# Kernel tuning notes

Hardware: AMD Instinct MI355X
Metric: run time of the kernel (lower is better)

Reference implementation:

```python
import jax, jax.numpy as jnp
import numpy as np
from jax.scipy.optimize import minimize

LAMDA = 0.01        # lamda default in MI()
N_DOMAINS = 2       # domain_label is binary (source/target)
MAXITER = 50        # BFGS iteration budget (torchmin l-bfgs analogue)


def _sq_dists(A, B):
    # squared euclidean pairwise distances == torch.cdist(A, B, p=2) ** 2
    an = jnp.sum(A * A, axis=-1)
    bn = jnp.sum(B * B, axis=-1)
    return an[:, None] + bn[None, :] - 2.0 * (A @ B.T)


def _median_sigma(sf):
    # sigma = median of nonzero squared pairwise source distances.
    # With continuous features the only zeros are the diagonal, so mask it.
    pd = jnp.maximum(_sq_dists(sf, sf), 0.0)
    pd = jnp.where(jnp.eye(pd.shape[0], dtype=bool), jnp.nan, pd)
    return jnp.nanmedian(pd)


def _build(sf, tf, y, l):
    # Gaussian kernel masked by class agreement, plus domain one-hots.
    sigma = _median_sigma(sf)
    X = jnp.concatenate([sf, tf], axis=0)              # [N, d]
    D = _sq_dists(X, X)                                 # [N, N]
    Deltay = (y[:, None] == y[None, :]).astype(X.dtype)
    K_W = jnp.exp(-D / sigma) * Deltay                  # [N, N]
    onehot = jax.nn.one_hot(l[:, 0], N_DOMAINS, dtype=X.dtype)  # [N, 2]
    KD = K_W * (onehot @ onehot.T)                      # K_W * Deltal
    w = jnp.sum(onehot, axis=0) / X.shape[0]            # domain counts / N
    return K_W, KD, onehot, w


def _div(theta, K_W, KD, onehot, w):
    # mean((K_W*Deltal) @ theta) - mean(exp((theta*K_W) @ Deltal - 1))
    # Deltal = onehot @ onehot.T (rank-2), so the second NxN @ NxN matmul
    # collapses to A = K_W @ (theta[:,None]*onehot) with column weights w.
    term1 = jnp.mean(KD @ theta)
    A = K_W @ (theta[:, None] * onehot)                 # [N, 2]
    term2 = jnp.mean(jnp.exp(A - 1.0) @ w)
    return term1 - term2


def _solve_theta(K_W, KD, onehot, w):
    N = K_W.shape[0]
    obj = lambda th: -_div(th, K_W, KD, onehot, w) + LAMDA * (th @ th)
    res = minimize(obj, jnp.zeros((N,), K_W.dtype), method="BFGS",
                   options={"maxiter": MAXITER})
    return res.x


def setup_inputs() -> dict:
    key = jax.random.key(0)
    k1, k2, k3, k4 = jax.random.split(key, 4)
    B, d, n_class = 2048, 256, 31
    source_features = jax.random.normal(k1, (B, d), dtype=jnp.float32)
    target_features = jax.random.normal(k2, (B, d), dtype=jnp.float32)
    y = jax.random.randint(k3, (2 * B,), 0, n_class, dtype=jnp.int32)
    l = jax.random.randint(k4, (2 * B, 1), 0, N_DOMAINS, dtype=jnp.int32)
    return {"source_features": source_features, "target_features": target_features,
            "y": y, "l": l}


def reference(source_features, target_features, y, l):
    K_W, KD, onehot, w = _build(source_features, target_features, y, l)
    theta_hat = _solve_theta(K_W, KD, onehot, w)
    return _div(theta_hat, K_W, KD, onehot, w)
```

## Files before the change

kernel.cpp:

```cpp
#include <hip/hip_runtime.h>
#include <math.h>

#define N_TOT   4096
#define N_SRC   2048
#define DIMF    256
#define NCLASS  31
#define LAMBDA  0.01f

#define K_TRI1  1048063LL
#define K_TRI2  1048064LL

#define WS_ACC    0
#define WS_HIST0  64
#define WS_HISTA  16448
#define WS_HISTB  32832
#define WS_H2A    49216
#define WS_H2B    50240
#define WS_STATE  51264
#define WS_TICK   51520
#define WS_META   52288
#define WS_SCAL   52800
#define ZERO_BYTES 53248
#define WS_PERM   53248
#define WS_XN     69632
#define WS_DS     1048576
#define WS_KBLK   17825792

#define MAXW 224
#define MAXM 112
#define WPAD 116

__device__ __forceinline__ float bf2f(unsigned short h) {
  return __uint_as_float(((unsigned)h) << 16);
}

__device__ __forceinline__ float wredF(float v) {
#pragma unroll
  for (int o = 1; o < 64; o <<= 1) v += __shfl_xor(v, o, 64);
  return v;
}

__device__ __forceinline__ double blockReduceSum(double v, double* red) {
#pragma unroll
  for (int o = 32; o > 0; o >>= 1) v += __shfl_down(v, o, 64);
  int w = threadIdx.x >> 6, lane = threadIdx.x & 63;
  __syncthreads();
  if (lane == 0) red[w] = v;
  __syncthreads();
  return red[0] + red[1] + red[2] + red[3];
}

__device__ __forceinline__ void blockReduceSumMax(double s, double mx, double* red,
                                                  double& os, double& om) {
#pragma unroll
  for (int o = 32; o > 0; o >>= 1) {
    s += __shfl_down(s, o, 64);
    double u = __shfl_down(mx, o, 64);
    mx = fmax(mx, u);
  }
  int w = threadIdx.x >> 6, lane = threadIdx.x & 63;
  __syncthreads();
  if (lane == 0) { red[w] = s; red[4 + w] = mx; }
  __syncthreads();
  os = red[0] + red[1] + red[2] + red[3];
  om = fmax(fmax(red[4], red[5]), fmax(red[6], red[7]));
}

__device__ void scan_find(const unsigned* hist, int nbins, long long k, unsigned* shOut, int tid) {
  __shared__ long long tsum[256];
  int per = nbins / 256;
  long long s = 0;
  for (int q = 0; q < per; q++) s += hist[tid * per + q];
  tsum[tid] = s;
  __syncthreads();
  long long acc = s;
  for (int off = 1; off < 256; off <<= 1) {
    long long add = (tid >= off) ? tsum[tid - off] : 0;
    __syncthreads();
    acc += add;
    tsum[tid] = acc;
    __syncthreads();
  }
  long long run = acc - s;
  for (int q = 0; q < per; q++) {
    unsigned c = hist[tid * per + q];
    if (k >= run && k < run + (long long)c) { shOut[0] = (unsigned)(tid * per + q); shOut[1] = (unsigned)(k - run); }
    run += c;
  }
  __syncthreads();
}

__global__ __launch_bounds__(256) void xn_kernel(const float* __restrict__ sf,
                                                 const float* __restrict__ tf,
                                                 float* __restrict__ xn,
                                                 uint4* __restrict__ wsz) {
  if (blockIdx.x == 0) {
    uint4 z; z.x = 0; z.y = 0; z.z = 0; z.w = 0;
    for (int q = threadIdx.x; q < ZERO_BYTES / 16; q += 256) wsz[q] = z;
  }
  int wid = threadIdx.x >> 6, lane = threadIdx.x & 63;
  int row = blockIdx.x * 4 + wid;
  const float* src = (row < N_SRC) ? (sf + (size_t)row * DIMF) : (tf + (size_t)(row - N_SRC) * DIMF);
  float4 v = ((const float4*)src)[lane];
  float s = v.x * v.x + v.y * v.y + v.z * v.z + v.w * v.w;
#pragma unroll
  for (int o = 32; o > 0; o >>= 1) s += __shfl_down(s, o, 64);
  if (lane == 0) xn[row] = s;
}

__global__ __launch_bounds__(256) void dist_k(const float* __restrict__ sf,
                                              const float* __restrict__ xn,
                                              float* __restrict__ Ds,
                                              unsigned* __restrict__ h) {
  __shared__ float As[16][68];
  __shared__ float Bs[16][68];
  __shared__ unsigned lh[2][4096];
  const int tx = threadIdx.x, ty = threadIdx.y;
  const int tid = ty * 16 + tx;
  const int par = tid & 1;
  for (int q = tid; q < 8192; q += 256) lh[q >> 12][q & 4095] = 0;
  int b = blockIdx.x;
  int by = (int)((sqrtf(8.f * (float)b + 1.f) - 1.f) * 0.5f);
  while ((by + 1) * (by + 2) / 2 <= b) ++by;
  while (by * (by + 1) / 2 > b) --by;
  int bx = b - by * (by + 1) / 2;
  const int R = by * 64, C = bx * 64;
  const int si = tid >> 2, sq = tid & 3;
  float4 va = ((const float4*)(sf + (size_t)(R + si) * 256 + 0))[sq];
  float4 vb = ((const float4*)(sf + (size_t)(C + si) * 256 + 0))[sq];
  float acc[4][4] = {};
  for (int kc = 0; kc < 256; kc += 16) {
    As[sq * 4 + 0][si] = va.x; As[sq * 4 + 1][si] = va.y; As[sq * 4 + 2][si] = va.z; As[sq * 4 + 3][si] = va.w;
    Bs[sq * 4 + 0][si] = vb.x; Bs[sq * 4 + 1][si] = vb.y; Bs[sq * 4 + 2][si] = vb.z; Bs[sq * 4 + 3][si] = vb.w;
    __syncthreads();
    if (kc + 16 < 256) {
      va = ((const float4*)(sf + (size_t)(R + si) * 256 + kc + 16))[sq];
      vb = ((const float4*)(sf + (size_t)(C + si) * 256 + kc + 16))[sq];
    }
#pragma unroll
    for (int k = 0; k < 16; k++) {
      float4 a = *(const float4*)&As[k][ty * 4];
      float4 b2 = *(const float4*)&Bs[k][tx * 4];
      acc[0][0] += a.x * b2.x; acc[0][1] += a.x * b2.y; acc[0][2] += a.x * b2.z; acc[0][3] += a.x * b2.w;
      acc[1][0] += a.y * b2.x; acc[1][1] += a.y * b2.y; acc[1][2] += a.y * b2.z; acc[1][3] += a.y * b2.w;
      acc[2][0] += a.z * b2.x; acc[2][1] += a.z * b2.y; acc[2][2] += a.z * b2.z; acc[2][3] += a.z * b2.w;
      acc[3][0] += a.w * b2.x; acc[3][1] += a.w * b2.y; acc[3][2] += a.w * b2.z; acc[3][3] += a.w * b2.w;
    }
    __syncthreads();
  }
  int jbase = C + tx * 4;
  float xnj0 = xn[jbase + 0], xnj1 = xn[jbase + 1], xnj2 = xn[jbase + 2], xnj3 = xn[jbase + 3];
#pragma unroll
  for (int r = 0; r < 4; r++) {
    int i = R + ty * 4 + r;
    float xni = xn[i];
    float v[4];
    v[0] = fmaxf(xni + xnj0 - 2.f * acc[r][0], 0.f);
    v[1] = fmaxf(xni + xnj1 - 2.f * acc[r][1], 0.f);
    v[2] = fmaxf(xni + xnj2 - 2.f * acc[r][2], 0.f);
    v[3] = fmaxf(xni + xnj3 - 2.f * acc[r][3], 0.f);
    if (jbase + 3 < i) {
      float4 o; o.x = v[0]; o.y = v[1]; o.z = v[2]; o.w = v[3];
      ((float4*)&Ds[(size_t)i * 2048 + jbase])[0] = o;
      atomicAdd(&lh[par][__float_as_uint(v[0]) >> 20], 1u);
      atomicAdd(&lh[par][__float_as_uint(v[1]) >> 20], 1u);
      atomicAdd(&lh[par][__float_as_uint(v[2]) >> 20], 1u);
      atomicAdd(&lh[par][__float_as_uint(v[3]) >> 20], 1u);
    } else {
#pragma unroll
      for (int k = 0; k < 4; k++) {
        if (jbase + k < i) {
          Ds[(size_t)i * 2048 + jbase + k] = v[k];
          atomicAdd(&lh[par][__float_as_uint(v[k]) >> 20], 1u);
        }
      }
    }
  }
  __syncthreads();
  for (int q = tid; q < 4096; q += 256) {
    unsigned v = lh[0][q] + lh[1][q];
    if (v) atomicAdd(&h[q], v);
  }
}

__global__ __launch_bounds__(256) void scan0_k(const unsigned* __restrict__ h, unsigned* __restrict__ st) {
  __shared__ unsigned r0[2];
  __shared__ unsigned r1[2];
  scan_find(h, 4096, K_TRI1, r0, threadIdx.x);
  scan_find(h, 4096, K_TRI2, r1, threadIdx.x);
  if (threadIdx.x == 0) { st[0] = r0[0]; st[1] = r0[1]; st[2] = r1[0]; st[3] = r1[1]; }
}

__global__ __launch_bounds__(256) void hist1_k(const float* __restrict__ Ds, const unsigned* __restrict__ st,
                                               unsigned* __restrict__ hA, unsigned* __restrict__ hB) {
  __shared__ unsigned lA[4096];
  __shared__ unsigned lB[4096];
  for (int i = threadIdx.x; i < 4096; i += 256) { lA[i] = 0; lB[i] = 0; }
  __syncthreads();
  unsigned s0 = st[0], s1 = st[2];
  int gw = (blockIdx.x * 256 + threadIdx.x) >> 6;
  int lane = threadIdx.x & 63;
  const float* row = Ds + (size_t)gw * 2048;
  for (int j = lane; j < gw; j += 64) {
    unsigned u = __float_as_uint(row[j]);
    unsigned hi = u >> 20, mid = (u >> 8) & 0xFFFu;
    if (hi == s0) atomicAdd(&lA[mid], 1u);
    if (hi == s1) atomicAdd(&lB[mid], 1u);
  }
  __syncthreads();
  for (int i = threadIdx.x; i < 4096; i += 256) {
    if (lA[i]) atomicAdd(&hA[i], lA[i]);
    if (lB[i]) atomicAdd(&hB[i], lB[i]);
  }
}

__global__ __launch_bounds__(256) void scan1_k(const unsigned* __restrict__ hA, const unsigned* __restrict__ hB,
                                               unsigned* __restrict__ st) {
  __shared__ unsigned r0[2];
  __shared__ unsigned r1[2];
  long long kA = (long long)st[1];
  long long kB = (long long)st[3];
  scan_find(hA, 4096, kA, r0, threadIdx.x);
  scan_find(hB, 4096, kB, r1, threadIdx.x);
  if (threadIdx.x == 0) { st[4] = r0[0]; st[5] = r0[1]; st[6] = r1[0]; st[7] = r1[1]; }
}

__global__ __launch_bounds__(256) void hist2_k(const float* __restrict__ Ds, const unsigned* __restrict__ st,
                                               unsigned* __restrict__ hA, unsigned* __restrict__ hB) {
  __shared__ unsigned lA[256];
  __shared__ unsigned lB[256];
  lA[threadIdx.x] = 0; lB[threadIdx.x] = 0;
  __syncthreads();
  unsigned p0 = (st[0] << 12) | st[4];
  unsigned p1 = (st[2] << 12) | st[6];
  int gw = (blockIdx.x * 256 + threadIdx.x) >> 6;
  int lane = threadIdx.x & 63;
  const float* row = Ds + (size_t)gw * 2048;
  for (int j = lane; j < gw; j += 64) {
    unsigned u = __float_as_uint(row[j]);
    unsigned pre = u >> 8;
    if (pre == p0) atomicAdd(&lA[u & 0xFFu], 1u);
    if (pre == p1) atomicAdd(&lB[u & 0xFFu], 1u);
  }
  __syncthreads();
  if (lA[threadIdx.x]) atomicAdd(&hA[threadIdx.x], lA[threadIdx.x]);
  if (lB[threadIdx.x]) atomicAdd(&hB[threadIdx.x], lB[threadIdx.x]);
}

__global__ __launch_bounds__(256) void scan2b_k(const unsigned* __restrict__ hA, const unsigned* __restrict__ hB,
                                                const unsigned* __restrict__ st, float* __restrict__ scal,
                                                const int* __restrict__ y, const int* __restrict__ l,
                                                int* __restrict__ perm, int* __restrict__ meta) {
  int tid = threadIdx.x;
  __shared__ unsigned r0[2];
  __shared__ unsigned r1[2];
  scan_find(hA, 256, (long long)st[5], r0, tid);
  scan_find(hB, 256, (long long)st[7], r1, tid);
  if (tid == 0) {
    unsigned v1 = (st[0] << 20) | (st[4] << 8) | r0[0];
    unsigned v2 = (st[2] << 20) | (st[6] << 8) | r1[0];
    scal[0] = 0.5f * (__uint_as_float(v1) + __uint_as_float(v2));
  }
  __shared__ unsigned cl[64];
  __shared__ unsigned bs2[64];
  __shared__ unsigned cur[64];
  if (tid < 64) cl[tid] = 0;
  __syncthreads();
  for (int i = tid; i < N_TOT; i += 256) atomicAdd(&cl[y[i] * 2 + l[i]], 1u);
  __syncthreads();
  if (tid == 0) {
    unsigned run = 0;
    for (int b2 = 0; b2 < 62; b2++) { bs2[b2] = run; run += cl[b2]; }
    unsigned run2 = 0, cnt0 = 0;
    for (int c = 0; c < NCLASS; c++) {
      int n = (int)(cl[2 * c] + cl[2 * c + 1]);
      meta[c] = n; meta[32 + c] = (int)cl[2 * c]; meta[64 + c] = (int)bs2[2 * c];
      meta[96 + c] = (int)run2; run2 += (unsigned)(n * n);
      cnt0 += cl[2 * c];
    }
    scal[1] = (float)((double)cnt0 / (4096.0 * 4096.0));
    scal[2] = (float)((double)(N_TOT - cnt0) / (4096.0 * 4096.0));
  }
  __syncthreads();
  if (tid < 64) cur[tid] = bs2[tid];
  __syncthreads();
  for (int i = tid; i < N_TOT; i += 256) {
    int b2 = y[i] * 2 + l[i];
    unsigned pos = atomicAdd(&cur[b2], 1u);
    perm[pos] = i;
  }
}

__global__ __launch_bounds__(256) void build_k(const float* __restrict__ sf, const float* __restrict__ tf,
                                               const float* __restrict__ xn, const int* __restrict__ perm,
                                               const int* __restrict__ meta, const float* __restrict__ scal,
                                               float* __restrict__ gK) {
  const int c = blockIdx.z;
  const int n = meta[c];
  const int cs = meta[64 + c];
  const int bo = meta[96 + c];
  const int T = (n + 15) >> 4;
  int b = blockIdx.x;
  if (b >= T * (T + 1) / 2) return;
  int by = (int)((sqrtf(8.f * (float)b + 1.f) - 1.f) * 0.5f);
  while ((by + 1) * (by + 2) / 2 <= b) ++by;
  while (by * (by + 1) / 2 > b) --by;
  int bx = b - by * (by + 1) / 2;
  const int i0 = by * 16, j0 = bx * 16;
  const int tx = threadIdx.x, ty = threadIdx.y;
  __shared__ float As[16][260];
  __shared__ float Bs[16][260];
  __shared__ float ot[16][17];
  __shared__ int ra[16];
  __shared__ int rb[16];
  int tid = ty * 16 + tx;
  if (tid < 16) { int il = i0 + tid; ra[tid] = (il < n) ? perm[cs + il] : -1; }
  else if (tid < 32) { int jl = j0 + tid - 16; rb[tid - 16] = (jl < n) ? perm[cs + jl] : -1; }
  __syncthreads();
  for (int e = tid; e < 1024; e += 256) {
    int r = e >> 6, q = e & 63;
    int g = ra[r];
    if (g >= 0) {
      const float* src = (g < N_SRC) ? (sf + (size_t)g * DIMF) : (tf + (size_t)(g - N_SRC) * DIMF);
      ((float4*)&As[r][q * 4])[0] = ((const float4*)src)[q];
    }
    int g2 = rb[r];
    if (g2 >= 0) {
      const float* src = (g2 < N_SRC) ? (sf + (size_t)g2 * DIMF) : (tf + (size_t)(g2 - N_SRC) * DIMF);
      ((float4*)&Bs[r][q * 4])[0] = ((const float4*)src)[q];
    }
  }
  __syncthreads();
  int il = i0 + ty, jl = j0 + tx;
  float val = 0.f;
  if (il < n && jl < n) {
    float dot = 0.f;
    const float4* a4 = (const float4*)&As[ty][0];
    const float4* b4 = (const float4*)&Bs[tx][0];
#pragma unroll 16
    for (int q = 0; q < 64; q++) {
      float4 a = a4[q], b2 = b4[q];
      dot += a.x * b2.x + a.y * b2.y + a.z * b2.z + a.w * b2.w;
    }
    int gi = ra[ty], gj = rb[tx];
    float d = xn[gi] + xn[gj] - 2.f * dot;
    val = expf(-d / scal[0]);
    gK[(size_t)bo + (size_t)il * n + jl] = val;
  }
  ot[ty][tx] = val;
  __syncthreads();
  if (by != bx) {
    int il2 = j0 + ty, jl2 = i0 + tx;
    if (il2 < n && jl2 < n) gK[(size_t)bo + (size_t)il2 * n + jl2] = ot[tx][ty];
  }
}

__global__ __launch_bounds__(256) void solver_k(const float* __restrict__ gK, const int* __restrict__ meta,
                                                const float* __restrict__ scal, double* __restrict__ acc,
                                                unsigned* __restrict__ tick, float* __restrict__ out) {
  const int c = blockIdx.x >> 1, d = blockIdx.x & 1;
  const int n = meta[c];
  const int m0 = meta[32 + c];
  const int m = d ? (n - m0) : m0;
  const int c0 = d ? m0 : 0;
  const int bo = meta[96 + c];
  const float gamma = scal[1 + d];
  const int tid = threadIdx.x;
  const int wv = tid >> 6, lane = tid & 63;

  __shared__ unsigned short Wl[MAXW * WPAD];
  __shared__ float pS[4 * MAXM];
  __shared__ float pD[4 * MAXM];
  __shared__ float Av[MAXW];
  __shared__ float Sv[MAXW];
  __shared__ float Uv[MAXW];
  __shared__ float Bq[MAXW];
  __shared__ float bc[MAXM];
  __shared__ float gv[MAXM];
  __shared__ float dgv[MAXM];
  __shared__ alignas(16) float th[128];
  __shared__ alignas(16) float pv[128];
  __shared__ alignas(16) float xv[128];
  __shared__ double red[16];
  __shared__ double gds[2];
  __shared__ int cgst[2];

  const float* K = gK + bo;
  const int st = n;
  const int mp2 = (m + 1) & ~1;
  const int mp4 = (m + 3) & ~3;
  const int iw0 = (n * wv) >> 2, iw1 = (n * (wv + 1)) >> 2;
  const int rq = tid >> 2, ql = tid & 3;

  for (int i = rq; i < n; i += 64) {
    const float* Kr = K + (size_t)i * st + c0;
    unsigned short* Wr = Wl + i * WPAD;
    for (int j = ql; j < m; j += 4) {
      unsigned u = __float_as_uint(Kr[j]);
      u += 0x7fffu + ((u >> 16) & 1u);
      Wr[j] = (unsigned short)(u >> 16);
    }
    if (ql == 0) for (int j = m; j < mp4; j++) Wr[j] = 0;
  }
  for (int j = rq; j < m; j += 64) {
    const float* Kr = K + (size_t)(c0 + j) * st + c0;
    float s = 0.f;
    for (int r = ql; r < m; r += 4) s += Kr[r];
    s += __shfl_xor(s, 1, 64);
    s += __shfl_xor(s, 2, 64);
    if (ql == 0) bc[j] = s * (1.0f / 4096.0f);
  }
  __syncthreads();
  for (int j = tid; j < 128; j += 256) { th[j] = 0.f; pv[j] = 0.f; xv[j] = 0.f; }
  __syncthreads();

  for (int it = 0; it < 25; it++) {
    double o = 0.0;
    if (it == 0) {
      const float s0c = gamma * expf(-1.f);
      for (int i = tid; i < n; i += 256) { Av[i] = 0.f; Sv[i] = s0c; o += (double)s0c; }
    } else {
      for (int i = tid; i < n; i += 256) {
        const unsigned short* Wr = Wl + i * WPAD;
        float a = 0.f;
#pragma unroll 4
        for (int j = 0; j < mp4; j += 4) {
          unsigned long long u = *(const unsigned long long*)(Wr + j);
          float4 t4 = *(const float4*)(th + j);
          unsigned lo = (unsigned)u, hi = (unsigned)(u >> 32);
          a += __uint_as_float(lo << 16) * t4.x
             + __uint_as_float(lo & 0xffff0000u) * t4.y
             + __uint_as_float(hi << 16) * t4.z
             + __uint_as_float(hi & 0xffff0000u) * t4.w;
        }
        Av[i] = a;
        float si = gamma * expf(fminf(a - 1.f, 30.f));
        Sv[i] = si; o += (double)si;
      }
      for (int j = tid; j < m; j += 256) {
        float t_ = th[j];
        o += (double)(-bc[j] * t_ + LAMBDA * t_ * t_);
      }
    }
    __syncthreads();
    if (it == 0) {
      for (int j = lane; j < m; j += 64) {
        const unsigned short* Wc = Wl + j;
        float s_ = 0.f, ds_ = 0.f;
        int i = iw0;
        for (; i + 3 < iw1; i += 4) {
          float w0 = bf2f(Wc[(i + 0) * WPAD]), w1 = bf2f(Wc[(i + 1) * WPAD]);
          float w2 = bf2f(Wc[(i + 2) * WPAD]), w3 = bf2f(Wc[(i + 3) * WPAD]);
          float a0 = w0 * Sv[i], a1 = w1 * Sv[i + 1], a2 = w2 * Sv[i + 2], a3 = w3 * Sv[i + 3];
          s_ += a0 + a1 + a2 + a3;
          ds_ += a0 * w0 + a1 * w1 + a2 * w2 + a3 * w3;
        }
        for (; i < iw1; i++) { float w = bf2f(Wc[i * WPAD]); float a = w * Sv[i]; s_ += a; ds_ += a * w; }
        pS[wv * MAXM + j] = s_; pD[wv * MAXM + j] = ds_;
      }
    } else {
      for (int j = lane; j < m; j += 64) {
        const unsigned short* Wc = Wl + j;
        float s_ = 0.f;
        int i = iw0;
        for (; i + 3 < iw1; i += 4)
          s_ += bf2f(Wc[(i+0)*WPAD]) * Sv[i]   + bf2f(Wc[(i+1)*WPAD]) * Sv[i+1]
              + bf2f(Wc[(i+2)*WPAD]) * Sv[i+2] + bf2f(Wc[(i+3)*WPAD]) * Sv[i+3];
        for (; i < iw1; i++) s_ += bf2f(Wc[i * WPAD]) * Sv[i];
        pS[wv * MAXM + j] = s_;
      }
    }
    __syncthreads();
    double gm = 0.0;
    for (int j = tid; j < m; j += 256) {
      float s_ = pS[j] + pS[MAXM + j] + pS[2 * MAXM + j] + pS[3 * MAXM + j];
      if (it == 0) {
        float ds_ = pD[j] + pD[MAXM + j] + pD[2 * MAXM + j] + pD[3 * MAXM + j];
        dgv[j] = ds_ + 2.f * LAMBDA;
      }
      float g = s_ - bc[j] + 2.f * LAMBDA * th[j];
      gv[j] = g;
      double ag = fabs((double)g); if (ag > gm) gm = ag;
    }
    double obj, gmax;
    blockReduceSumMax(o, gm, red, obj, gmax);
    if (gmax < 1e-5) break;

    const float tolf = (it == 0) ? 1e-2f : ((it == 1) ? 1e-3f : 1e-4f);
    float p0 = 0.f, p1 = 0.f, r0 = 0.f, r1 = 0.f, z0 = 0.f, z1 = 0.f, x0 = 0.f, x1 = 0.f;
    float dg0 = 1.f, dg1 = 1.f, rzf = 0.f, rz0f = 0.f;
    double gtpacc = 0.0;
    const int j0 = lane, j1 = lane + 64;
    if (wv == 0) {
      if (j0 < m) { dg0 = dgv[j0]; r0 = -gv[j0]; z0 = r0 / dg0; }
      if (j1 < m) { dg1 = dgv[j1]; r1 = -gv[j1]; z1 = r1 / dg1; }
      p0 = z0; p1 = z1;
      rzf = wredF(r0 * z0 + r1 * z1);
      rz0f = rzf;
      pv[j0] = p0; pv[j1] = p1;
      if (lane == 0) cgst[0] = (rzf > 0.f) ? 0 : 1;
    }
    __syncthreads();
    for (int cg = 0; cg < 12; cg++) {
      if (cgst[0]) break;
      for (int i = tid; i < n; i += 256) {
        const unsigned short* Wr = Wl + i * WPAD;
        float a = 0.f;
#pragma unroll 4
        for (int j = 0; j < mp4; j += 4) {
          unsigned long long u = *(const unsigned long long*)(Wr + j);
          float4 t4 = *(const float4*)(pv + j);
          unsigned lo = (unsigned)u, hi = (unsigned)(u >> 32);
          a += __uint_as_float(lo << 16) * t4.x
             + __uint_as_float(lo & 0xffff0000u) * t4.y
             + __uint_as_float(hi << 16) * t4.z
             + __uint_as_float(hi & 0xffff0000u) * t4.w;
        }
        Uv[i] = a * Sv[i];
      }
      __syncthreads();
      for (int j = lane; j < m; j += 64) {
        const unsigned short* Wc = Wl + j;
        float q = 0.f;
        int i = iw0;
        for (; i + 3 < iw1; i += 4)
          q += bf2f(Wc[(i+0)*WPAD]) * Uv[i]   + bf2f(Wc[(i+1)*WPAD]) * Uv[i+1]
             + bf2f(Wc[(i+2)*WPAD]) * Uv[i+2] + bf2f(Wc[(i+3)*WPAD]) * Uv[i+3];
        for (; i < iw1; i++) q += bf2f(Wc[i * WPAD]) * Uv[i];
        pS[wv * MAXM + j] = q;
      }
      __syncthreads();
      if (wv == 0) {
        float q0 = 0.f, q1 = 0.f;
        if (j0 < m) q0 = pS[j0] + pS[MAXM + j0] + pS[2*MAXM + j0] + pS[3*MAXM + j0] + 2.f * LAMBDA * p0;
        if (j1 < m) q1 = pS[j1] + pS[MAXM + j1] + pS[2*MAXM + j1] + pS[3*MAXM + j1] + 2.f * LAMBDA * p1;
        float pq = wredF(p0 * q0 + p1 * q1);
        int stop = 0;
        if (!(pq > 0.f)) stop = 1;
        else {
          float alpha = rzf / pq;
          gtpacc += (double)alpha * (double)rzf;
          x0 += alpha * p0; x1 += alpha * p1;
          r0 -= alpha * q0; r1 -= alpha * q1;
          z0 = r0 / dg0;    z1 = r1 / dg1;
          float rzn = wredF(r0 * z0 + r1 * z1);
          if (rzn < tolf * rz0f || cg == 11) stop = 1;
          else {
            float beta = rzn / rzf;
            p0 = z0 + beta * p0; p1 = z1 + beta * p1;
            pv[j0] = p0; pv[j1] = p1;
            rzf = rzn;
          }
        }
        if (lane == 0) cgst[0] = stop;
      }
      __syncthreads();
    }
    if (wv == 0) {
      xv[j0] = x0; xv[j1] = x1;
      if (lane == 0) gds[0] = -gtpacc;
    }
    __syncthreads();
    double gtp = gds[0];
    if (!(gtp < 0.0)) break;

    float t = 1.f;
    if (-gtp >= 1e-4) {
      for (int i = tid; i < n; i += 256) {
        const unsigned short* Wr = Wl + i * WPAD;
        float a = 0.f;
#pragma unroll 4
        for (int j = 0; j < mp4; j += 4) {
          unsigned long long u = *(const unsigned long long*)(Wr + j);
          float4 t4 = *(const float4*)(xv + j);
          unsigned lo = (unsigned)u, hi = (unsigned)(u >> 32);
          a += __uint_as_float(lo << 16) * t4.x
             + __uint_as_float(lo & 0xffff0000u) * t4.y
             + __uint_as_float(hi << 16) * t4.z
             + __uint_as_float(hi & 0xffff0000u) * t4.w;
        }
        Bq[i] = a;
      }
      __syncthreads();
      for (int ls = 0; ls < 10; ls++) {
        double ol = 0.0;
        for (int i = tid; i < n; i += 256)
          ol += (double)(gamma * expf(fminf(Av[i] + t * Bq[i] - 1.f, 30.f)));
        for (int j = tid; j < m; j += 256) {
          float tj = th[j] + t * xv[j];
          ol += (double)(-bc[j] * tj + LAMBDA * tj * tj);
        }
        double ot2 = blockReduceSum(ol, red);
        if (ot2 <= obj + 1e-4 * (double)t * gtp) break;
        t *= 0.5f;
      }
    }
    for (int j = tid; j < mp2; j += 256) th[j] += t * xv[j];
    __syncthreads();
  }

  __syncthreads();
  for (int i = rq; i < n; i += 64) {
    const float* Kr = K + (size_t)i * st + c0;
    float a = 0.f;
#pragma unroll 4
    for (int j = ql; j < m; j += 4) a += th[j] * Kr[j];
    a += __shfl_xor(a, 1, 64);
    a += __shfl_xor(a, 2, 64);
    if (ql == 0) Av[i] = a;
  }
  __syncthreads();
  double t1l = 0.0, t2l = 0.0;
  for (int i = tid; i < n; i += 256) t2l += (double)(gamma * expf(fminf(Av[i] - 1.f, 30.f)));
  for (int j = tid; j < m; j += 256) t1l += (double)(bc[j] * th[j]);
  double t1 = blockReduceSum(t1l, red);
  double t2 = blockReduceSum(t2l, red);
  if (tid == 0) {
    atomicAdd(&acc[0], t1);
    atomicAdd(&acc[1], t2);
    __threadfence();
    unsigned old = __hip_atomic_fetch_add(&tick[0], 1u, __ATOMIC_ACQ_REL, __HIP_MEMORY_SCOPE_AGENT);
    if (old == 61u) {
      double a0 = __hip_atomic_load(&acc[0], __ATOMIC_RELAXED, __HIP_MEMORY_SCOPE_AGENT);
      double a1 = __hip_atomic_load(&acc[1], __ATOMIC_RELAXED, __HIP_MEMORY_SCOPE_AGENT);
      out[0] = (float)(a0 - a1);
    }
  }
}

extern "C" void kernel_launch(void* const* d_in, const int* in_sizes, int n_in,
                              void* d_out, int out_size, void* d_ws, size_t ws_size,
                              hipStream_t stream) {
  const float* sf = (const float*)d_in[0];
  const float* tf = (const float*)d_in[1];
  const int* y = (const int*)d_in[2];
  const int* l = (const int*)d_in[3];
  char* ws = (char*)d_ws;

  double*   acc    = (double*)(ws + WS_ACC);
  unsigned* hist0  = (unsigned*)(ws + WS_HIST0);
  unsigned* histA  = (unsigned*)(ws + WS_HISTA);
  unsigned* histB  = (unsigned*)(ws + WS_HISTB);
  unsigned* h2A    = (unsigned*)(ws + WS_H2A);
  unsigned* h2B    = (unsigned*)(ws + WS_H2B);
  unsigned* state  = (unsigned*)(ws + WS_STATE);
  unsigned* tick   = (unsigned*)(ws + WS_TICK);
  int*      meta   = (int*)(ws + WS_META);
  float*    scal   = (float*)(ws + WS_SCAL);
  int*      perm   = (int*)(ws + WS_PERM);
  float*    xnp    = (float*)(ws + WS_XN);
  float*    Ds     = (float*)(ws + WS_DS);
  float*    gK     = (float*)(ws + WS_KBLK);

  hipLaunchKernelGGL(xn_kernel, dim3(1024), dim3(256), 0, stream, sf, tf, xnp, (uint4*)ws);
  hipLaunchKernelGGL(dist_k, dim3(528), dim3(16, 16), 0, stream, sf, xnp, Ds, hist0);
  hipLaunchKernelGGL(scan0_k, dim3(1), dim3(256), 0, stream, hist0, state);
  hipLaunchKernelGGL(hist1_k, dim3(512), dim3(256), 0, stream, Ds, state, histA, histB);
  hipLaunchKernelGGL(scan1_k, dim3(1), dim3(256), 0, stream, histA, histB, state);
  hipLaunchKernelGGL(hist2_k, dim3(512), dim3(256), 0, stream, Ds, state, h2A, h2B);
  hipLaunchKernelGGL(scan2b_k, dim3(1), dim3(256), 0, stream, h2A, h2B, state, scal, y, l, perm, meta);
  hipLaunchKernelGGL(build_k, dim3(105, 1, NCLASS), dim3(16, 16), 0, stream, sf, tf, xnp, perm, meta, scal, gK);
  hipLaunchKernelGGL(solver_k, dim3(62), dim3(256), 0, stream, gK, meta, scal, acc, tick, (float*)d_out);
}
```

Baseline: 206.9 us.

## Use 64x64 register-tiled Gram blocks in build and wave-local row ranges in solver

The per-class kernel build now computes 64x64 output tiles, with each thread accumulating a 4x4 register tile over k-chunks of 16 staged in shared memory. The previous version used 16x16 tiles with one dot product per thread over the full 256-dim rows. The grid shrinks from 105 to 10 triangle blocks per class. In the solver, each wave now computes the rows it later reduces over (iw0..iw1), so two block-wide __syncthreads per CG iteration and per outer iteration can be dropped. This relies on the wave-local row ranges being exactly the ones each wave consumes, and 10 blocks per class must still cover T(T+1)/2 for the largest class.

```diff
diff --git a/kernel.cpp b/kernel.cpp
--- a/kernel.cpp
+++ b/kernel.cpp
@@ -299,59 +299,82 @@
   const int n = meta[c];
   const int cs = meta[64 + c];
   const int bo = meta[96 + c];
-  const int T = (n + 15) >> 4;
+  const int T = (n + 63) >> 6;
   int b = blockIdx.x;
   if (b >= T * (T + 1) / 2) return;
   int by = (int)((sqrtf(8.f * (float)b + 1.f) - 1.f) * 0.5f);
   while ((by + 1) * (by + 2) / 2 <= b) ++by;
   while (by * (by + 1) / 2 > b) --by;
   int bx = b - by * (by + 1) / 2;
-  const int i0 = by * 16, j0 = bx * 16;
+  const int i0 = by * 64, j0 = bx * 64;
   const int tx = threadIdx.x, ty = threadIdx.y;
-  __shared__ float As[16][260];
-  __shared__ float Bs[16][260];
-  __shared__ float ot[16][17];
-  __shared__ int ra[16];
-  __shared__ int rb[16];
-  int tid = ty * 16 + tx;
-  if (tid < 16) { int il = i0 + tid; ra[tid] = (il < n) ? perm[cs + il] : -1; }
-  else if (tid < 32) { int jl = j0 + tid - 16; rb[tid - 16] = (jl < n) ? perm[cs + jl] : -1; }
-  __syncthreads();
-  for (int e = tid; e < 1024; e += 256) {
-    int r = e >> 6, q = e & 63;
-    int g = ra[r];
-    if (g >= 0) {
-      const float* src = (g < N_SRC) ? (sf + (size_t)g * DIMF) : (tf + (size_t)(g - N_SRC) * DIMF);
-      ((float4*)&As[r][q * 4])[0] = ((const float4*)src)[q];
-    }
-    int g2 = rb[r];
-    if (g2 >= 0) {
-      const float* src = (g2 < N_SRC) ? (sf + (size_t)g2 * DIMF) : (tf + (size_t)(g2 - N_SRC) * DIMF);
-      ((float4*)&Bs[r][q * 4])[0] = ((const float4*)src)[q];
-    }
-  }
-  __syncthreads();
-  int il = i0 + ty, jl = j0 + tx;
-  float val = 0.f;
-  if (il < n && jl < n) {
-    float dot = 0.f;
-    const float4* a4 = (const float4*)&As[ty][0];
-    const float4* b4 = (const float4*)&Bs[tx][0];
-#pragma unroll 16
-    for (int q = 0; q < 64; q++) {
-      float4 a = a4[q], b2 = b4[q];
-      dot += a.x * b2.x + a.y * b2.y + a.z * b2.z + a.w * b2.w;
-    }
-    int gi = ra[ty], gj = rb[tx];
-    float d = xn[gi] + xn[gj] - 2.f * dot;
-    val = expf(-d / scal[0]);
-    gK[(size_t)bo + (size_t)il * n + jl] = val;
-  }
-  ot[ty][tx] = val;
-  __syncthreads();
+  const int tid = ty * 16 + tx;
+  __shared__ float As[16][68];
+  __shared__ float Bs[16][68];
+  __shared__ float vt[64][65];
+  __shared__ int ra[64];
+  __shared__ int rb[64];
+  __shared__ float xna[64];
+  __shared__ float xnb[64];
+  if (tid < 64) {
+    int il = i0 + tid;
+    int g = (il < n) ? perm[cs + il] : perm[cs];
+    ra[tid] = g; xna[tid] = xn[g];
+  } else if (tid < 128) {
+    int q = tid - 64;
+    int jl = j0 + q;
+    int g = (jl < n) ? perm[cs + jl] : perm[cs];
+    rb[q] = g; xnb[q] = xn[g];
+  }
+  __syncthreads();
+  const int si = tid >> 2, sq = tid & 3;
+  int ga = ra[si], gb = rb[si];
+  const float* pa = (ga < N_SRC) ? (sf + (size_t)ga * DIMF) : (tf + (size_t)(ga - N_SRC) * DIMF);
+  const float* pb = (gb < N_SRC) ? (sf + (size_t)gb * DIMF) : (tf + (size_t)(gb - N_SRC) * DIMF);
+  float4 va = ((const float4*)pa)[sq];
+  float4 vb = ((const float4*)pb)[sq];
+  float acc[4][4] = {};
+  for (int kc = 0; kc < 256; kc += 16) {
+    As[sq * 4 + 0][si] = va.x; As[sq * 4 + 1][si] = va.y; As[sq * 4 + 2][si] = va.z; As[sq * 4 + 3][si] = va.w;
+    Bs[sq * 4 + 0][si] = vb.x; Bs[sq * 4 + 1][si] = vb.y; Bs[sq * 4 + 2][si] = vb.z; Bs[sq * 4 + 3][si] = vb.w;
+    __syncthreads();
+    if (kc + 16 < 256) {
+      va = ((const float4*)(pa + kc + 16))[sq];
+      vb = ((const float4*)(pb + kc + 16))[sq];
+    }
+#pragma unroll
+    for (int k = 0; k < 16; k++) {
+      float4 a = *(const float4*)&As[k][ty * 4];
+      float4 b2 = *(const float4*)&Bs[k][tx * 4];
+      acc[0][0] += a.x * b2.x; acc[0][1] += a.x * b2.y; acc[0][2] += a.x * b2.z; acc[0][3] += a.x * b2.w;
+      acc[1][0] += a.y * b2.x; acc[1][1] += a.y * b2.y; acc[1][2] += a.y * b2.z; acc[1][3] += a.y * b2.w;
+      acc[2][0] += a.z * b2.x; acc[2][1] += a.z * b2.y; acc[2][2] += a.z * b2.z; acc[2][3] += a.z * b2.w;
+      acc[3][0] += a.w * b2.x; acc[3][1] += a.w * b2.y; acc[3][2] += a.w * b2.z; acc[3][3] += a.w * b2.w;
+    }
+    __syncthreads();
+  }
+  const float inv_sig = 1.f / scal[0];
+#pragma unroll
+  for (int r = 0; r < 4; r++) {
+    float xni = xna[ty * 4 + r];
+#pragma unroll
+    for (int q2 = 0; q2 < 4; q2++) {
+      float d_ = xni + xnb[tx * 4 + q2] - 2.f * acc[r][q2];
+      vt[ty * 4 + r][tx * 4 + q2] = expf(-d_ * inv_sig);
+    }
+  }
+  __syncthreads();
+  for (int e = tid; e < 4096; e += 256) {
+    int r = e >> 6, q2 = e & 63;
+    int il = i0 + r, jl = j0 + q2;
+    if (il < n && jl < n) gK[(size_t)bo + (size_t)il * n + jl] = vt[r][q2];
+  }
   if (by != bx) {
-    int il2 = j0 + ty, jl2 = i0 + tx;
-    if (il2 < n && jl2 < n) gK[(size_t)bo + (size_t)il2 * n + jl2] = ot[tx][ty];
+    for (int e = tid; e < 4096; e += 256) {
+      int r = e >> 6, q2 = e & 63;
+      int il = j0 + r, jl = i0 + q2;
+      if (il < n && jl < n) gK[(size_t)bo + (size_t)il * n + jl] = vt[q2][r];
+    }
   }
 }
 
@@ -418,9 +441,9 @@
     double o = 0.0;
     if (it == 0) {
       const float s0c = gamma * expf(-1.f);
-      for (int i = tid; i < n; i += 256) { Av[i] = 0.f; Sv[i] = s0c; o += (double)s0c; }
+      for (int i = iw0 + lane; i < iw1; i += 64) { Av[i] = 0.f; Sv[i] = s0c; o += (double)s0c; }
     } else {
-      for (int i = tid; i < n; i += 256) {
+      for (int i = iw0 + lane; i < iw1; i += 64) {
         const unsigned short* Wr = Wl + i * WPAD;
         float a = 0.f;
 #pragma unroll 4
@@ -442,7 +465,6 @@
         o += (double)(-bc[j] * t_ + LAMBDA * t_ * t_);
       }
     }
-    __syncthreads();
     if (it == 0) {
       for (int j = lane; j < m; j += 64) {
         const unsigned short* Wc = Wl + j;
@@ -503,7 +525,7 @@
     __syncthreads();
     for (int cg = 0; cg < 12; cg++) {
       if (cgst[0]) break;
-      for (int i = tid; i < n; i += 256) {
+      for (int i = iw0 + lane; i < iw1; i += 64) {
         const unsigned short* Wr = Wl + i * WPAD;
         float a = 0.f;
 #pragma unroll 4
@@ -518,7 +540,6 @@
         }
         Uv[i] = a * Sv[i];
       }
-      __syncthreads();
       for (int j = lane; j < m; j += 64) {
         const unsigned short* Wc = Wl + j;
         float q = 0.f;
@@ -659,6 +680,6 @@
   hipLaunchKernelGGL(scan1_k, dim3(1), dim3(256), 0, stream, histA, histB, state);
   hipLaunchKernelGGL(hist2_k, dim3(512), dim3(256), 0, stream, Ds, state, h2A, h2B);
   hipLaunchKernelGGL(scan2b_k, dim3(1), dim3(256), 0, stream, h2A, h2B, state, scal, y, l, perm, meta);
-  hipLaunchKernelGGL(build_k, dim3(105, 1, NCLASS), dim3(16, 16), 0, stream, sf, tf, xnp, perm, meta, scal, gK);
+  hipLaunchKernelGGL(build_k, dim3(10, 1, NCLASS), dim3(16, 16), 0, stream, sf, tf, xnp, perm, meta, scal, gK);
   hipLaunchKernelGGL(solver_k, dim3(62), dim3(256), 0, stream, gK, meta, scal, acc, tick, (float*)d_out);
 }
```

New measurement: 215.2 us. 4.0% more time.

## Use single-wavefront blocks with 8x8 register tiles in distance kernel

Applied to the files above, without the earlier changes.

Restructures the source-distance GEMM kernel from 256-thread blocks with 4x4 per-thread tiles to one 64-thread wavefront per block with 8x8 per-thread tiles. Because a block is now a single wavefront, the block barriers around the shared-memory staging are removed. Each thread now loads a whole 16-float slice of one row per step, and the histogram clear uses vector stores. The aim is more arithmetic per shared-memory load and no barrier cost. The trade-off is far fewer resident waves to hide memory latency, and per-thread global loads that are strided by a full row.

```diff
diff --git a/kernel.cpp b/kernel.cpp
--- a/kernel.cpp
+++ b/kernel.cpp
@@ -108,76 +108,95 @@
   if (lane == 0) xn[row] = s;
 }
 
-__global__ __launch_bounds__(256) void dist_k(const float* __restrict__ sf,
-                                              const float* __restrict__ xn,
-                                              float* __restrict__ Ds,
-                                              unsigned* __restrict__ h) {
+__global__ __launch_bounds__(64) void dist_k(const float* __restrict__ sf,
+                                             const float* __restrict__ xn,
+                                             float* __restrict__ Ds,
+                                             unsigned* __restrict__ h) {
   __shared__ float As[16][68];
   __shared__ float Bs[16][68];
   __shared__ unsigned lh[2][4096];
-  const int tx = threadIdx.x, ty = threadIdx.y;
-  const int tid = ty * 16 + tx;
+  const int tid = threadIdx.x;
   const int par = tid & 1;
-  for (int q = tid; q < 8192; q += 256) lh[q >> 12][q & 4095] = 0;
+  {
+    uint4 z; z.x = 0; z.y = 0; z.z = 0; z.w = 0;
+    for (int q = tid; q < 2048; q += 64) ((uint4*)lh)[q] = z;
+  }
   int b = blockIdx.x;
   int by = (int)((sqrtf(8.f * (float)b + 1.f) - 1.f) * 0.5f);
   while ((by + 1) * (by + 2) / 2 <= b) ++by;
   while (by * (by + 1) / 2 > b) --by;
   int bx = b - by * (by + 1) / 2;
   const int R = by * 64, C = bx * 64;
-  const int si = tid >> 2, sq = tid & 3;
-  float4 va = ((const float4*)(sf + (size_t)(R + si) * 256 + 0))[sq];
-  float4 vb = ((const float4*)(sf + (size_t)(C + si) * 256 + 0))[sq];
-  float acc[4][4] = {};
+  const int ty = tid >> 3, tx = tid & 7;
+  const float* pa = sf + (size_t)(R + tid) * DIMF;
+  const float* pb = sf + (size_t)(C + tid) * DIMF;
+  float4 va0 = ((const float4*)pa)[0], va1 = ((const float4*)pa)[1];
+  float4 va2 = ((const float4*)pa)[2], va3 = ((const float4*)pa)[3];
+  float4 vb0 = ((const float4*)pb)[0], vb1 = ((const float4*)pb)[1];
+  float4 vb2 = ((const float4*)pb)[2], vb3 = ((const float4*)pb)[3];
+  float acc[8][8] = {};
   for (int kc = 0; kc < 256; kc += 16) {
-    As[sq * 4 + 0][si] = va.x; As[sq * 4 + 1][si] = va.y; As[sq * 4 + 2][si] = va.z; As[sq * 4 + 3][si] = va.w;
-    Bs[sq * 4 + 0][si] = vb.x; Bs[sq * 4 + 1][si] = vb.y; Bs[sq * 4 + 2][si] = vb.z; Bs[sq * 4 + 3][si] = vb.w;
-    __syncthreads();
+    As[0][tid] = va0.x;  As[1][tid] = va0.y;  As[2][tid] = va0.z;  As[3][tid] = va0.w;
+    As[4][tid] = va1.x;  As[5][tid] = va1.y;  As[6][tid] = va1.z;  As[7][tid] = va1.w;
+    As[8][tid] = va2.x;  As[9][tid] = va2.y;  As[10][tid] = va2.z; As[11][tid] = va2.w;
+    As[12][tid] = va3.x; As[13][tid] = va3.y; As[14][tid] = va3.z; As[15][tid] = va3.w;
+    Bs[0][tid] = vb0.x;  Bs[1][tid] = vb0.y;  Bs[2][tid] = vb0.z;  Bs[3][tid] = vb0.w;
+    Bs[4][tid] = vb1.x;  Bs[5][tid] = vb1.y;  Bs[6][tid] = vb1.z;  Bs[7][tid] = vb1.w;
+    Bs[8][tid] = vb2.x;  Bs[9][tid] = vb2.y;  Bs[10][tid] = vb2.z; Bs[11][tid] = vb2.w;
+    Bs[12][tid] = vb3.x; Bs[13][tid] = vb3.y; Bs[14][tid] = vb3.z; Bs[15][tid] = vb3.w;
     if (kc + 16 < 256) {
-      va = ((const float4*)(sf + (size_t)(R + si) * 256 + kc + 16))[sq];
-      vb = ((const float4*)(sf + (size_t)(C + si) * 256 + kc + 16))[sq];
+      const float* qa = pa + kc + 16;
+      const float* qb = pb + kc + 16;
+      va0 = ((const float4*)qa)[0]; va1 = ((const float4*)qa)[1];
+      va2 = ((const float4*)qa)[2]; va3 = ((const float4*)qa)[3];
+      vb0 = ((const float4*)qb)[0]; vb1 = ((const float4*)qb)[1];
+      vb2 = ((const float4*)qb)[2]; vb3 = ((const float4*)qb)[3];
     }
 #pragma unroll
     for (int k = 0; k < 16; k++) {
-      float4 a = *(const float4*)&As[k][ty * 4];
-      float4 b2 = *(const float4*)&Bs[k][tx * 4];
-      acc[0][0] += a.x * b2.x; acc[0][1] += a.x * b2.y; acc[0][2] += a.x * b2.z; acc[0][3] += a.x * b2.w;
-      acc[1][0] += a.y * b2.x; acc[1][1] += a.y * b2.y; acc[1][2] += a.y * b2.z; acc[1][3] += a.y * b2.w;
-      acc[2][0] += a.z * b2.x; acc[2][1] += a.z * b2.y; acc[2][2] += a.z * b2.z; acc[2][3] += a.z * b2.w;
-      acc[3][0] += a.w * b2.x; acc[3][1] += a.w * b2.y; acc[3][2] += a.w * b2.z; acc[3][3] += a.w * b2.w;
-    }
-    __syncthreads();
-  }
-  int jbase = C + tx * 4;
-  float xnj0 = xn[jbase + 0], xnj1 = xn[jbase + 1], xnj2 = xn[jbase + 2], xnj3 = xn[jbase + 3];
-#pragma unroll
-  for (int r = 0; r < 4; r++) {
-    int i = R + ty * 4 + r;
+      float4 a0 = *(const float4*)&As[k][ty * 8];
+      float4 a1 = *(const float4*)&As[k][ty * 8 + 4];
+      float4 b0 = *(const float4*)&Bs[k][tx * 8];
+      float4 b1 = *(const float4*)&Bs[k][tx * 8 + 4];
+      float av[8] = {a0.x, a0.y, a0.z, a0.w, a1.x, a1.y, a1.z, a1.w};
+      float bv[8] = {b0.x, b0.y, b0.z, b0.w, b1.x, b1.y, b1.z, b1.w};
+#pragma unroll
+      for (int r = 0; r < 8; r++)
+#pragma unroll
+        for (int q = 0; q < 8; q++)
+          acc[r][q] += av[r] * bv[q];
+    }
+  }
+  const int jbase = C + tx * 8;
+  float xnj[8];
+#pragma unroll
+  for (int q = 0; q < 8; q++) xnj[q] = xn[jbase + q];
+#pragma unroll
+  for (int r = 0; r < 8; r++) {
+    int i = R + ty * 8 + r;
     float xni = xn[i];
-    float v[4];
-    v[0] = fmaxf(xni + xnj0 - 2.f * acc[r][0], 0.f);
-    v[1] = fmaxf(xni + xnj1 - 2.f * acc[r][1], 0.f);
-    v[2] = fmaxf(xni + xnj2 - 2.f * acc[r][2], 0.f);
-    v[3] = fmaxf(xni + xnj3 - 2.f * acc[r][3], 0.f);
-    if (jbase + 3 < i) {
-      float4 o; o.x = v[0]; o.y = v[1]; o.z = v[2]; o.w = v[3];
-      ((float4*)&Ds[(size_t)i * 2048 + jbase])[0] = o;
-      atomicAdd(&lh[par][__float_as_uint(v[0]) >> 20], 1u);
-      atomicAdd(&lh[par][__float_as_uint(v[1]) >> 20], 1u);
-      atomicAdd(&lh[par][__float_as_uint(v[2]) >> 20], 1u);
-      atomicAdd(&lh[par][__float_as_uint(v[3]) >> 20], 1u);
+    float v[8];
+#pragma unroll
+    for (int q = 0; q < 8; q++) v[q] = fmaxf(xni + xnj[q] - 2.f * acc[r][q], 0.f);
+    if (jbase + 7 < i) {
+      float4 o0; o0.x = v[0]; o0.y = v[1]; o0.z = v[2]; o0.w = v[3];
+      float4 o1; o1.x = v[4]; o1.y = v[5]; o1.z = v[6]; o1.w = v[7];
+      ((float4*)&Ds[(size_t)i * 2048 + jbase])[0] = o0;
+      ((float4*)&Ds[(size_t)i * 2048 + jbase])[1] = o1;
+#pragma unroll
+      for (int q = 0; q < 8; q++) atomicAdd(&lh[par][__float_as_uint(v[q]) >> 20], 1u);
     } else {
 #pragma unroll
-      for (int k = 0; k < 4; k++) {
-        if (jbase + k < i) {
-          Ds[(size_t)i * 2048 + jbase + k] = v[k];
-          atomicAdd(&lh[par][__float_as_uint(v[k]) >> 20], 1u);
+      for (int q = 0; q < 8; q++) {
+        if (jbase + q < i) {
+          Ds[(size_t)i * 2048 + jbase + q] = v[q];
+          atomicAdd(&lh[par][__float_as_uint(v[q]) >> 20], 1u);
         }
       }
     }
   }
   __syncthreads();
-  for (int q = tid; q < 4096; q += 256) {
+  for (int q = tid; q < 4096; q += 64) {
     unsigned v = lh[0][q] + lh[1][q];
     if (v) atomicAdd(&h[q], v);
   }
@@ -653,7 +672,7 @@
   float*    gK     = (float*)(ws + WS_KBLK);
 
   hipLaunchKernelGGL(xn_kernel, dim3(1024), dim3(256), 0, stream, sf, tf, xnp, (uint4*)ws);
-  hipLaunchKernelGGL(dist_k, dim3(528), dim3(16, 16), 0, stream, sf, xnp, Ds, hist0);
+  hipLaunchKernelGGL(dist_k, dim3(528), dim3(64), 0, stream, sf, xnp, Ds, hist0);
   hipLaunchKernelGGL(scan0_k, dim3(1), dim3(256), 0, stream, hist0, state);
   hipLaunchKernelGGL(hist1_k, dim3(512), dim3(256), 0, stream, Ds, state, histA, histB);
   hipLaunchKernelGGL(scan1_k, dim3(1), dim3(256), 0, stream, histA, histB, state);
```

New measurement: 226.6 us. 9.5% more time.

## Track line-search matvec incrementally from CG iterates and move class bucketing to xn kernel

Applied to the files above, without the earlier changes.

The solver no longer recomputes W·x with a full bf16 matvec before the line search. It accumulates alpha·(W p) per row during CG, using linearity, and keeps the A vector in a register instead of shared memory. This assumes n ≤ 256 so each thread owns at most one row. Separately, the class/domain counting and permutation work moves from the serial single-block scan2b kernel into block 0 of the xn kernel, taking it off the critical path but lengthening that one block.

```diff
diff --git a/kernel.cpp b/kernel.cpp
--- a/kernel.cpp
+++ b/kernel.cpp
@@ -93,12 +93,46 @@
 __global__ __launch_bounds__(256) void xn_kernel(const float* __restrict__ sf,
                                                  const float* __restrict__ tf,
                                                  float* __restrict__ xn,
-                                                 uint4* __restrict__ wsz) {
+                                                 uint4* __restrict__ wsz,
+                                                 const int* __restrict__ y,
+                                                 const int* __restrict__ l,
+                                                 int* __restrict__ perm,
+                                                 int* __restrict__ meta,
+                                                 float* __restrict__ scal) {
+  __shared__ unsigned cl[64];
+  __shared__ unsigned bs2[64];
+  __shared__ unsigned cur[64];
+  const int tid = threadIdx.x;
   if (blockIdx.x == 0) {
     uint4 z; z.x = 0; z.y = 0; z.z = 0; z.w = 0;
-    for (int q = threadIdx.x; q < ZERO_BYTES / 16; q += 256) wsz[q] = z;
-  }
-  int wid = threadIdx.x >> 6, lane = threadIdx.x & 63;
+    for (int q = tid; q < ZERO_BYTES / 16; q += 256) wsz[q] = z;
+    if (tid < 64) cl[tid] = 0;
+    __syncthreads();
+    for (int i = tid; i < N_TOT; i += 256) atomicAdd(&cl[y[i] * 2 + l[i]], 1u);
+    __syncthreads();
+    if (tid == 0) {
+      unsigned run = 0;
+      for (int b2 = 0; b2 < 62; b2++) { bs2[b2] = run; run += cl[b2]; }
+      unsigned run2 = 0, cnt0 = 0;
+      for (int c = 0; c < NCLASS; c++) {
+        int n = (int)(cl[2 * c] + cl[2 * c + 1]);
+        meta[c] = n; meta[32 + c] = (int)cl[2 * c]; meta[64 + c] = (int)bs2[2 * c];
+        meta[96 + c] = (int)run2; run2 += (unsigned)(n * n);
+        cnt0 += cl[2 * c];
+      }
+      scal[1] = (float)((double)cnt0 / (4096.0 * 4096.0));
+      scal[2] = (float)((double)(N_TOT - cnt0) / (4096.0 * 4096.0));
+    }
+    __syncthreads();
+    if (tid < 64) cur[tid] = bs2[tid];
+    __syncthreads();
+    for (int i = tid; i < N_TOT; i += 256) {
+      int b2 = y[i] * 2 + l[i];
+      unsigned pos = atomicAdd(&cur[b2], 1u);
+      perm[pos] = i;
+    }
+  }
+  int wid = tid >> 6, lane = tid & 63;
   int row = blockIdx.x * 4 + wid;
   const float* src = (row < N_SRC) ? (sf + (size_t)row * DIMF) : (tf + (size_t)(row - N_SRC) * DIMF);
   float4 v = ((const float4*)src)[lane];
@@ -248,9 +282,7 @@
 }
 
 __global__ __launch_bounds__(256) void scan2b_k(const unsigned* __restrict__ hA, const unsigned* __restrict__ hB,
-                                                const unsigned* __restrict__ st, float* __restrict__ scal,
-                                                const int* __restrict__ y, const int* __restrict__ l,
-                                                int* __restrict__ perm, int* __restrict__ meta) {
+                                                const unsigned* __restrict__ st, float* __restrict__ scal) {
   int tid = threadIdx.x;
   __shared__ unsigned r0[2];
   __shared__ unsigned r1[2];
@@ -260,34 +292,6 @@
     unsigned v1 = (st[0] << 20) | (st[4] << 8) | r0[0];
     unsigned v2 = (st[2] << 20) | (st[6] << 8) | r1[0];
     scal[0] = 0.5f * (__uint_as_float(v1) + __uint_as_float(v2));
-  }
-  __shared__ unsigned cl[64];
-  __shared__ unsigned bs2[64];
-  __shared__ unsigned cur[64];
-  if (tid < 64) cl[tid] = 0;
-  __syncthreads();
-  for (int i = tid; i < N_TOT; i += 256) atomicAdd(&cl[y[i] * 2 + l[i]], 1u);
-  __syncthreads();
-  if (tid == 0) {
-    unsigned run = 0;
-    for (int b2 = 0; b2 < 62; b2++) { bs2[b2] = run; run += cl[b2]; }
-    unsigned run2 = 0, cnt0 = 0;
-    for (int c = 0; c < NCLASS; c++) {
-      int n = (int)(cl[2 * c] + cl[2 * c + 1]);
-      meta[c] = n; meta[32 + c] = (int)cl[2 * c]; meta[64 + c] = (int)bs2[2 * c];
-      meta[96 + c] = (int)run2; run2 += (unsigned)(n * n);
-      cnt0 += cl[2 * c];
-    }
-    scal[1] = (float)((double)cnt0 / (4096.0 * 4096.0));
-    scal[2] = (float)((double)(N_TOT - cnt0) / (4096.0 * 4096.0));
-  }
-  __syncthreads();
-  if (tid < 64) cur[tid] = bs2[tid];
-  __syncthreads();
-  for (int i = tid; i < N_TOT; i += 256) {
-    int b2 = y[i] * 2 + l[i];
-    unsigned pos = atomicAdd(&cur[b2], 1u);
-    perm[pos] = i;
   }
 }
 
@@ -374,7 +378,6 @@
   __shared__ float Av[MAXW];
   __shared__ float Sv[MAXW];
   __shared__ float Uv[MAXW];
-  __shared__ float Bq[MAXW];
   __shared__ float bc[MAXM];
   __shared__ float gv[MAXM];
   __shared__ float dgv[MAXM];
@@ -383,6 +386,7 @@
   __shared__ alignas(16) float xv[128];
   __shared__ double red[16];
   __shared__ double gds[2];
+  __shared__ float alf_s[2];
   __shared__ int cgst[2];
 
   const float* K = gK + bo;
@@ -414,11 +418,14 @@
   for (int j = tid; j < 128; j += 256) { th[j] = 0.f; pv[j] = 0.f; xv[j] = 0.f; }
   __syncthreads();
 
+  float av_r = 0.f;
+
   for (int it = 0; it < 25; it++) {
     double o = 0.0;
     if (it == 0) {
       const float s0c = gamma * expf(-1.f);
-      for (int i = tid; i < n; i += 256) { Av[i] = 0.f; Sv[i] = s0c; o += (double)s0c; }
+      av_r = 0.f;
+      for (int i = tid; i < n; i += 256) { Sv[i] = s0c; o += (double)s0c; }
     } else {
       for (int i = tid; i < n; i += 256) {
         const unsigned short* Wr = Wl + i * WPAD;
@@ -433,7 +440,7 @@
              + __uint_as_float(hi << 16) * t4.z
              + __uint_as_float(hi & 0xffff0000u) * t4.w;
         }
-        Av[i] = a;
+        av_r = a;
         float si = gamma * expf(fminf(a - 1.f, 30.f));
         Sv[i] = si; o += (double)si;
       }
@@ -489,6 +496,7 @@
     const float tolf = (it == 0) ? 1e-2f : ((it == 1) ? 1e-3f : 1e-4f);
     float p0 = 0.f, p1 = 0.f, r0 = 0.f, r1 = 0.f, z0 = 0.f, z1 = 0.f, x0 = 0.f, x1 = 0.f;
     float dg0 = 1.f, dg1 = 1.f, rzf = 0.f, rz0f = 0.f;
+    float bq = 0.f, wp = 0.f;
     double gtpacc = 0.0;
     const int j0 = lane, j1 = lane + 64;
     if (wv == 0) {
@@ -498,11 +506,13 @@
       rzf = wredF(r0 * z0 + r1 * z1);
       rz0f = rzf;
       pv[j0] = p0; pv[j1] = p1;
-      if (lane == 0) cgst[0] = (rzf > 0.f) ? 0 : 1;
-    }
-    __syncthreads();
+      if (lane == 0) { cgst[0] = (rzf > 0.f) ? 0 : 1; cgst[1] = 0; }
+    }
+    __syncthreads();
+    bool brk = false;
     for (int cg = 0; cg < 12; cg++) {
-      if (cgst[0]) break;
+      if (cgst[1]) bq += alf_s[0] * wp;
+      if (cgst[0]) { brk = true; break; }
       for (int i = tid; i < n; i += 256) {
         const unsigned short* Wr = Wl + i * WPAD;
         float a = 0.f;
@@ -516,6 +526,7 @@
              + __uint_as_float(hi << 16) * t4.z
              + __uint_as_float(hi & 0xffff0000u) * t4.w;
         }
+        wp = a;
         Uv[i] = a * Sv[i];
       }
       __syncthreads();
@@ -536,13 +547,16 @@
         if (j1 < m) q1 = pS[j1] + pS[MAXM + j1] + pS[2*MAXM + j1] + pS[3*MAXM + j1] + 2.f * LAMBDA * p1;
         float pq = wredF(p0 * q0 + p1 * q1);
         int stop = 0;
-        if (!(pq > 0.f)) stop = 1;
-        else {
+        if (!(pq > 0.f)) {
+          stop = 1;
+          if (lane == 0) cgst[1] = 0;
+        } else {
           float alpha = rzf / pq;
           gtpacc += (double)alpha * (double)rzf;
           x0 += alpha * p0; x1 += alpha * p1;
           r0 -= alpha * q0; r1 -= alpha * q1;
           z0 = r0 / dg0;    z1 = r1 / dg1;
+          if (lane == 0) { alf_s[0] = alpha; cgst[1] = 1; }
           float rzn = wredF(r0 * z0 + r1 * z1);
           if (rzn < tolf * rz0f || cg == 11) stop = 1;
           else {
@@ -556,6 +570,7 @@
       }
       __syncthreads();
     }
+    if (!brk && cgst[1]) bq += alf_s[0] * wp;
     if (wv == 0) {
       xv[j0] = x0; xv[j1] = x1;
       if (lane == 0) gds[0] = -gtpacc;
@@ -566,26 +581,9 @@
 
     float t = 1.f;
     if (-gtp >= 1e-4) {
-      for (int i = tid; i < n; i += 256) {
-        const unsigned short* Wr = Wl + i * WPAD;
-        float a = 0.f;
-#pragma unroll 4
-        for (int j = 0; j < mp4; j += 4) {
-          unsigned long long u = *(const unsigned long long*)(Wr + j);
-          float4 t4 = *(const float4*)(xv + j);
-          unsigned lo = (unsigned)u, hi = (unsigned)(u >> 32);
-          a += __uint_as_float(lo << 16) * t4.x
-             + __uint_as_float(lo & 0xffff0000u) * t4.y
-             + __uint_as_float(hi << 16) * t4.z
-             + __uint_as_float(hi & 0xffff0000u) * t4.w;
-        }
-        Bq[i] = a;
-      }
-      __syncthreads();
       for (int ls = 0; ls < 10; ls++) {
         double ol = 0.0;
-        for (int i = tid; i < n; i += 256)
-          ol += (double)(gamma * expf(fminf(Av[i] + t * Bq[i] - 1.f, 30.f)));
+        if (tid < n) ol += (double)(gamma * expf(fminf(av_r + t * bq - 1.f, 30.f)));
         for (int j = tid; j < m; j += 256) {
           float tj = th[j] + t * xv[j];
           ol += (double)(-bc[j] * tj + LAMBDA * tj * tj);
@@ -652,13 +650,13 @@
   float*    Ds     = (float*)(ws + WS_DS);
   float*    gK     = (float*)(ws + WS_KBLK);
 
-  hipLaunchKernelGGL(xn_kernel, dim3(1024), dim3(256), 0, stream, sf, tf, xnp, (uint4*)ws);
+  hipLaunchKernelGGL(xn_kernel, dim3(1024), dim3(256), 0, stream, sf, tf, xnp, (uint4*)ws, y, l, perm, meta, scal);
   hipLaunchKernelGGL(dist_k, dim3(528), dim3(16, 16), 0, stream, sf, xnp, Ds, hist0);
   hipLaunchKernelGGL(scan0_k, dim3(1), dim3(256), 0, stream, hist0, state);
   hipLaunchKernelGGL(hist1_k, dim3(512), dim3(256), 0, stream, Ds, state, histA, histB);
   hipLaunchKernelGGL(scan1_k, dim3(1), dim3(256), 0, stream, histA, histB, state);
   hipLaunchKernelGGL(hist2_k, dim3(512), dim3(256), 0, stream, Ds, state, h2A, h2B);
-  hipLaunchKernelGGL(scan2b_k, dim3(1), dim3(256), 0, stream, h2A, h2B, state, scal, y, l, perm, meta);
+  hipLaunchKernelGGL(scan2b_k, dim3(1), dim3(256), 0, stream, h2A, h2B, state, scal);
   hipLaunchKernelGGL(build_k, dim3(105, 1, NCLASS), dim3(16, 16), 0, stream, sf, tf, xnp, perm, meta, scal, gK);
   hipLaunchKernelGGL(solver_k, dim3(62), dim3(256), 0, stream, gK, meta, scal, acc, tick, (float*)d_out);
 }
```

Measured after the change: 205.3 us, median of 2. About the same (-0.8%).
